# Kernel tuning notes

Measured on AMD Instinct MI355X. Metric: run time of the kernel, lower is better.

Reference implementation:

```python
import jax, jax.numpy as jnp
import numpy as np

RES = 64            # resolution -> RES*RES grid points
BW = 0.3            # kernel bandwidth
P = 2.0             # weight power
BOX = np.array([[-3.0, 3.0], [-3.0, 3.0]], dtype=np.float32)  # fixed_box [[min,max],[min,max]]


def _grid():
    # regular RES x RES grid over BOX, flattened to (M, 2)
    ax0 = np.linspace(BOX[0, 0], BOX[0, 1], RES, dtype=np.float32)
    ax1 = np.linspace(BOX[1, 0], BOX[1, 1], RES, dtype=np.float32)
    g0, g1 = np.meshgrid(ax0, ax1, indexing='ij')
    return jnp.asarray(np.stack([g0.ravel(), g1.ravel()], axis=-1))


def setup_inputs() -> dict:
    key = jax.random.key(0)
    k1, k2 = jax.random.split(key)
    Bs = jax.random.normal(k1, (4, 128, 16, 2), dtype=jnp.float32)  # birth corners (S,N,nB,2)
    Ds = jax.random.normal(k2, (4, 128, 16, 2), dtype=jnp.float32)  # death corners (S,N,nD,2)
    return {"Bs": Bs, "Ds": Ds}


def reference(Bs, Ds):
    # Bs: (S,N,nB,2) birth corners (pad with +inf), Ds: (S,N,nD,2) death corners (pad with -inf)
    x = _grid()                      # (M,2) grid points, M = RES*RES
    x0, x1 = x[:, 0], x[:, 1]

    # --- interleaving weights: dI0 per interval ---
    # pairwise relu(D - B).min(coords) -> max over (nB,nD); inf -> 0
    pw = jnp.min(jax.nn.relu(Ds[:, :, None, :, :] - Bs[:, :, :, None, :]), axis=-1)  # (S,N,nB,nD)
    w = jnp.max(pw, axis=(-1, -2))                                                   # (S,N)
    w = jnp.where(jnp.isfinite(w), w, 0.0)

    # --- distance from grid points to intervals ---
    # birth: min_k max_d (B[k,d] - x[d]); computed as elementwise max of the 2 coords
    db = jnp.min(
        jnp.maximum(Bs[..., 0][:, :, None, :] - x0[None, None, :, None],
                    Bs[..., 1][:, :, None, :] - x1[None, None, :, None]),
        axis=-1)                                                                     # (S,N,M)
    # death: min_k max_d (x[d] - D[k,d])
    dd = jnp.min(
        jnp.maximum(x0[None, None, :, None] - Ds[..., 0][:, :, None, :],
                    x1[None, None, :, None] - Ds[..., 1][:, :, None, :]),
        axis=-1)                                                                     # (S,N,M)
    dist = jnp.maximum(db, dd)                                                       # (S,N,M)

    # --- gaussian kernel, unsigned: exp(-0.5*(relu(dist)/bw)^2) * w^p, summed over intervals ---
    k = jnp.exp(-0.5 * (jax.nn.relu(dist) / BW) ** 2)
    img = jnp.sum(k * (w ** P)[:, :, None], axis=1)                                  # (S, M)
    return img  # flat vector per sample, shape (S, RES*RES)
```

## Files before the change

### kernel.cpp

```cpp
#include <hip/hip_runtime.h>
#include <math.h>

#define RES   64
#define NPTS  (RES * RES)
#define NB    4
#define NN    128
#define NP    16
#define STRIDE 36
#define PTS_PER_BLK 32
#define NCHUNK 32

__global__ __launch_bounds__(256)
void fused_kernel(const float* __restrict__ Bs, const float* __restrict__ Ds,
                  float* __restrict__ out) {
    __shared__ __align__(16) float sB[NN * STRIDE];
    __shared__ __align__(16) float sD[NN * STRIDE];
    __shared__ float sW2[NN];
    __shared__ float wp[2][NN];
    __shared__ float psum[NCHUNK][PTS_PER_BLK + 1];

    const int b    = blockIdx.x >> 7;
    const int pblk = blockIdx.x & 127;
    const int t    = threadIdx.x;

    const float4* gB = (const float4*)(Bs + (size_t)b * NN * NP * 2);
    const float4* gD = (const float4*)(Ds + (size_t)b * NN * NP * 2);
    #pragma unroll
    for (int r = 0; r < 4; ++r) {
        const int m   = t + 256 * r;
        const int off = (m >> 3) * STRIDE + (m & 7) * 4;
        *(float4*)(sB + off) = gB[m];
        *(float4*)(sD + off) = gD[m];
    }
    __syncthreads();

    {
        const int n  = t & 127;
        const int jh = t >> 7;
        const float4* B4 = (const float4*)(sB + n * STRIDE);
        const float4* D4 = (const float4*)(sD + n * STRIDE);
        float b0[NP], b1[NP];
        #pragma unroll
        for (int q = 0; q < 8; ++q) {
            const float4 f = B4[q];
            b0[2 * q] = f.x; b1[2 * q] = f.y;
            b0[2 * q + 1] = f.z; b1[2 * q + 1] = f.w;
        }
        float w = 0.0f;
        #pragma unroll
        for (int qq = 0; qq < 4; ++qq) {
            const float4 fd = D4[jh * 4 + qq];
            #pragma unroll
            for (int i = 0; i < NP; ++i) {
                w = fmaxf(w, fmaxf(fminf(fd.x - b0[i], fd.y - b1[i]), 0.0f));
                w = fmaxf(w, fmaxf(fminf(fd.z - b0[i], fd.w - b1[i]), 0.0f));
            }
        }
        wp[jh][n] = w;
    }
    __syncthreads();
    if (t < NN) {
        float wv = fmaxf(wp[0][t], wp[1][t]);
        if (!isfinite(wv)) wv = 0.0f;
        sW2[t] = wv * wv;
    }
    __syncthreads();

    const int g  = t & 7;
    const int c  = t >> 3;
    const int p0 = pblk * PTS_PER_BLK + 4 * g;
    const int i0 = p0 >> 6;
    const float x0 = -3.0f + 6.0f * (float)i0 / 63.0f;
    float x1v[4];
    #pragma unroll
    for (int j = 0; j < 4; ++j)
        x1v[j] = -3.0f + 6.0f * (float)((p0 + j) & 63) / 63.0f;

    const float cexp = -0.5f / (0.3f * 0.3f);
    float acc[4] = {0.0f, 0.0f, 0.0f, 0.0f};

    for (int k = 0; k < 4; ++k) {
        const int n = c + 32 * k;
        const float4* B4 = (const float4*)(sB + n * STRIDE);
        const float4* D4 = (const float4*)(sD + n * STRIDE);
        float db[4] = {1e30f, 1e30f, 1e30f, 1e30f};
        float dd[4] = {1e30f, 1e30f, 1e30f, 1e30f};
        #pragma unroll
        for (int q = 0; q < 8; ++q) {
            const float4 fb = B4[q];
            const float4 fd = D4[q];
            float s  = fb.x - x0;
            float sd = x0 - fd.x;
            #pragma unroll
            for (int j = 0; j < 4; ++j) {
                db[j] = fminf(db[j], fmaxf(s,  fb.y - x1v[j]));
                dd[j] = fminf(dd[j], fmaxf(sd, x1v[j] - fd.y));
            }
            s  = fb.z - x0;
            sd = x0 - fd.z;
            #pragma unroll
            for (int j = 0; j < 4; ++j) {
                db[j] = fminf(db[j], fmaxf(s,  fb.w - x1v[j]));
                dd[j] = fminf(dd[j], fmaxf(sd, x1v[j] - fd.w));
            }
        }
        const float w2n = sW2[n];
        #pragma unroll
        for (int j = 0; j < 4; ++j) {
            const float r = fmaxf(fmaxf(db[j], dd[j]), 0.0f);
            acc[j] = fmaf(__expf(cexp * r * r), w2n, acc[j]);
        }
    }

    #pragma unroll
    for (int j = 0; j < 4; ++j) psum[c][4 * g + j] = acc[j];
    __syncthreads();
    if (t < PTS_PER_BLK) {
        float s = 0.0f;
        #pragma unroll
        for (int q = 0; q < NCHUNK; ++q) s += psum[q][t];
        out[(size_t)b * NPTS + pblk * PTS_PER_BLK + t] = s;
    }
}

extern "C" void kernel_launch(void* const* d_in, const int* in_sizes, int n_in,
                              void* d_out, int out_size, void* d_ws, size_t ws_size,
                              hipStream_t stream) {
    const float* Bs = (const float*)d_in[0];
    const float* Ds = (const float*)d_in[1];
    float* out = (float*)d_out;
    fused_kernel<<<dim3(NB * (NPTS / PTS_PER_BLK)), dim3(256), 0, stream>>>(Bs, Ds, out);
}
```

Measured before the change: 62.45 us.

## Split weight computation into a pre-kernel and slice intervals across more blocks

The per-interval weights, which were recomputed redundantly in every block, are now computed once by a small separate kernel that also zeroes the output. The main kernel splits the 128 intervals of each sample into 4 slices, so it launches four times as many blocks, each loading only a quarter of the corner data into shared memory. Partial sums are combined with atomicAdd into global memory. This removes redundant weight computation and raises parallelism, at the cost of an extra launch, atomics, and a dependency on workspace memory.

```diff
diff --git a/kernel.cpp b/kernel.cpp
--- a/kernel.cpp
+++ b/kernel.cpp
@@ -8,66 +8,65 @@
 #define NP    16
 #define STRIDE 36
 #define PTS_PER_BLK 32
-#define NCHUNK 32
+#define NSLICE 4
+#define NCOMP_BLK 32
 
-__global__ __launch_bounds__(256)
-void fused_kernel(const float* __restrict__ Bs, const float* __restrict__ Ds,
-                  float* __restrict__ out) {
-    __shared__ __align__(16) float sB[NN * STRIDE];
-    __shared__ __align__(16) float sD[NN * STRIDE];
-    __shared__ float sW2[NN];
-    __shared__ float wp[2][NN];
-    __shared__ float psum[NCHUNK][PTS_PER_BLK + 1];
+__global__ __launch_bounds__(64)
+void w2_kernel(const float* __restrict__ Bs, const float* __restrict__ Ds,
+               float* __restrict__ w2, float* __restrict__ out) {
+    const int tid = blockIdx.x * 64 + threadIdx.x;
 
-    const int b    = blockIdx.x >> 7;
-    const int pblk = blockIdx.x & 127;
-    const int t    = threadIdx.x;
+    #pragma unroll
+    for (int k = 0; k < 32; ++k) out[tid + 512 * k] = 0.0f;
 
-    const float4* gB = (const float4*)(Bs + (size_t)b * NN * NP * 2);
-    const float4* gD = (const float4*)(Ds + (size_t)b * NN * NP * 2);
+    const float4* B4 = (const float4*)Bs + (size_t)tid * 8;
+    const float4* D4 = (const float4*)Ds + (size_t)tid * 8;
+    float b0[NP], b1[NP], d0[NP], d1[NP];
     #pragma unroll
-    for (int r = 0; r < 4; ++r) {
-        const int m   = t + 256 * r;
-        const int off = (m >> 3) * STRIDE + (m & 7) * 4;
-        *(float4*)(sB + off) = gB[m];
-        *(float4*)(sD + off) = gD[m];
+    for (int q = 0; q < 8; ++q) {
+        float4 f = B4[q];
+        b0[2*q] = f.x; b1[2*q] = f.y; b0[2*q+1] = f.z; b1[2*q+1] = f.w;
+        f = D4[q];
+        d0[2*q] = f.x; d1[2*q] = f.y; d0[2*q+1] = f.z; d1[2*q+1] = f.w;
+    }
+    float w = 0.0f;
+    #pragma unroll
+    for (int j = 0; j < NP; ++j) {
+        #pragma unroll
+        for (int i = 0; i < NP; ++i)
+            w = fmaxf(w, fminf(d0[j] - b0[i], d1[j] - b1[i]));
+    }
+    if (!isfinite(w)) w = 0.0f;
+    w2[tid] = w * w;
+}
+
+__global__ __launch_bounds__(256, 8)
+void main_kernel(const float* __restrict__ Bs, const float* __restrict__ Ds,
+                 const float* __restrict__ w2, float* __restrict__ out) {
+    __shared__ __align__(16) float sB[NCOMP_BLK * STRIDE];
+    __shared__ __align__(16) float sD[NCOMP_BLK * STRIDE];
+    __shared__ float psum[NCOMP_BLK][PTS_PER_BLK + 1];
+
+    const int bid   = blockIdx.x;
+    const int b     = bid >> 9;
+    const int pblk  = (bid >> 2) & 127;
+    const int slice = bid & 3;
+    const int t     = threadIdx.x;
+
+    {
+        const int comp0 = b * NN + slice * NCOMP_BLK;
+        const float4* gB = (const float4*)Bs + (size_t)comp0 * 8;
+        const float4* gD = (const float4*)Ds + (size_t)comp0 * 8;
+        const int off = (t >> 3) * STRIDE + (t & 7) * 4;
+        *(float4*)(sB + off) = gB[t];
+        *(float4*)(sD + off) = gD[t];
     }
     __syncthreads();
 
-    {
-        const int n  = t & 127;
-        const int jh = t >> 7;
-        const float4* B4 = (const float4*)(sB + n * STRIDE);
-        const float4* D4 = (const float4*)(sD + n * STRIDE);
-        float b0[NP], b1[NP];
-        #pragma unroll
-        for (int q = 0; q < 8; ++q) {
-            const float4 f = B4[q];
-            b0[2 * q] = f.x; b1[2 * q] = f.y;
-            b0[2 * q + 1] = f.z; b1[2 * q + 1] = f.w;
-        }
-        float w = 0.0f;
-        #pragma unroll
-        for (int qq = 0; qq < 4; ++qq) {
-            const float4 fd = D4[jh * 4 + qq];
-            #pragma unroll
-            for (int i = 0; i < NP; ++i) {
-                w = fmaxf(w, fmaxf(fminf(fd.x - b0[i], fd.y - b1[i]), 0.0f));
-                w = fmaxf(w, fmaxf(fminf(fd.z - b0[i], fd.w - b1[i]), 0.0f));
-            }
-        }
-        wp[jh][n] = w;
-    }
-    __syncthreads();
-    if (t < NN) {
-        float wv = fmaxf(wp[0][t], wp[1][t]);
-        if (!isfinite(wv)) wv = 0.0f;
-        sW2[t] = wv * wv;
-    }
-    __syncthreads();
+    const int g = t & 7;
+    const int c = t >> 3;
+    const float w2n = w2[b * NN + slice * NCOMP_BLK + c];
 
-    const int g  = t & 7;
-    const int c  = t >> 3;
     const int p0 = pblk * PTS_PER_BLK + 4 * g;
     const int i0 = p0 >> 6;
     const float x0 = -3.0f + 6.0f * (float)i0 / 63.0f;
@@ -76,50 +75,42 @@
     for (int j = 0; j < 4; ++j)
         x1v[j] = -3.0f + 6.0f * (float)((p0 + j) & 63) / 63.0f;
 
-    const float cexp = -0.5f / (0.3f * 0.3f);
-    float acc[4] = {0.0f, 0.0f, 0.0f, 0.0f};
-
-    for (int k = 0; k < 4; ++k) {
-        const int n = c + 32 * k;
-        const float4* B4 = (const float4*)(sB + n * STRIDE);
-        const float4* D4 = (const float4*)(sD + n * STRIDE);
-        float db[4] = {1e30f, 1e30f, 1e30f, 1e30f};
-        float dd[4] = {1e30f, 1e30f, 1e30f, 1e30f};
-        #pragma unroll
-        for (int q = 0; q < 8; ++q) {
-            const float4 fb = B4[q];
-            const float4 fd = D4[q];
-            float s  = fb.x - x0;
-            float sd = x0 - fd.x;
-            #pragma unroll
-            for (int j = 0; j < 4; ++j) {
-                db[j] = fminf(db[j], fmaxf(s,  fb.y - x1v[j]));
-                dd[j] = fminf(dd[j], fmaxf(sd, x1v[j] - fd.y));
-            }
-            s  = fb.z - x0;
-            sd = x0 - fd.z;
-            #pragma unroll
-            for (int j = 0; j < 4; ++j) {
-                db[j] = fminf(db[j], fmaxf(s,  fb.w - x1v[j]));
-                dd[j] = fminf(dd[j], fmaxf(sd, x1v[j] - fd.w));
-            }
-        }
-        const float w2n = sW2[n];
+    const float4* B4 = (const float4*)(sB + c * STRIDE);
+    const float4* D4 = (const float4*)(sD + c * STRIDE);
+    float db[4] = {1e30f, 1e30f, 1e30f, 1e30f};
+    float dd[4] = {1e30f, 1e30f, 1e30f, 1e30f};
+    #pragma unroll
+    for (int q = 0; q < 8; ++q) {
+        const float4 fb = B4[q];
+        const float4 fd = D4[q];
+        float s  = fb.x - x0;
+        float sd = x0 - fd.x;
         #pragma unroll
         for (int j = 0; j < 4; ++j) {
-            const float r = fmaxf(fmaxf(db[j], dd[j]), 0.0f);
-            acc[j] = fmaf(__expf(cexp * r * r), w2n, acc[j]);
+            db[j] = fminf(db[j], fmaxf(s,  fb.y - x1v[j]));
+            dd[j] = fminf(dd[j], fmaxf(sd, x1v[j] - fd.y));
+        }
+        s  = fb.z - x0;
+        sd = x0 - fd.z;
+        #pragma unroll
+        for (int j = 0; j < 4; ++j) {
+            db[j] = fminf(db[j], fmaxf(s,  fb.w - x1v[j]));
+            dd[j] = fminf(dd[j], fmaxf(sd, x1v[j] - fd.w));
         }
     }
+    const float cexp = -0.5f / (0.3f * 0.3f);
+    #pragma unroll
+    for (int j = 0; j < 4; ++j) {
+        const float r = fmaxf(fmaxf(db[j], dd[j]), 0.0f);
+        psum[c][4 * g + j] = __expf(cexp * r * r) * w2n;
+    }
+    __syncthreads();
 
-    #pragma unroll
-    for (int j = 0; j < 4; ++j) psum[c][4 * g + j] = acc[j];
-    __syncthreads();
     if (t < PTS_PER_BLK) {
-        float s = 0.0f;
+        float ssum = 0.0f;
         #pragma unroll
-        for (int q = 0; q < NCHUNK; ++q) s += psum[q][t];
-        out[(size_t)b * NPTS + pblk * PTS_PER_BLK + t] = s;
+        for (int q = 0; q < NCOMP_BLK; ++q) ssum += psum[q][t];
+        atomicAdd(&out[(size_t)b * NPTS + pblk * PTS_PER_BLK + t], ssum);
     }
 }
 
@@ -129,5 +120,8 @@
     const float* Bs = (const float*)d_in[0];
     const float* Ds = (const float*)d_in[1];
     float* out = (float*)d_out;
-    fused_kernel<<<dim3(NB * (NPTS / PTS_PER_BLK)), dim3(256), 0, stream>>>(Bs, Ds, out);
+    float* w2  = (float*)d_ws;
+
+    w2_kernel<<<dim3(8), dim3(64), 0, stream>>>(Bs, Ds, w2, out);
+    main_kernel<<<dim3(NB * 128 * NSLICE), dim3(256), 0, stream>>>(Bs, Ds, w2, out);
 }
```

Result: slower. 63.82 us (+2.2%).

## Use 1024-thread blocks with one interval per thread group and two-level reduction

Applied to the files above, without the earlier changes.

Block size grows from 256 to 1024 threads. Each group of 8 threads now owns one interval, so the per-thread loop over 4 intervals is gone. The weight computation is split across the 8 lanes and combined with xor shuffles, which removes a shared-memory round trip and one barrier. Partial sums go through a larger shared buffer with a two-level tree reduction. The aim is more parallelism and shorter per-thread serial chains, at the cost of more shared memory, more barriers on a large block, and lower occupancy limits per CU.

```diff
diff --git a/kernel.cpp b/kernel.cpp
--- a/kernel.cpp
+++ b/kernel.cpp
@@ -8,67 +8,57 @@
 #define NP    16
 #define STRIDE 36
 #define PTS_PER_BLK 32
-#define NCHUNK 32
 
-__global__ __launch_bounds__(256)
+__global__ __launch_bounds__(1024, 8)
 void fused_kernel(const float* __restrict__ Bs, const float* __restrict__ Ds,
                   float* __restrict__ out) {
     __shared__ __align__(16) float sB[NN * STRIDE];
     __shared__ __align__(16) float sD[NN * STRIDE];
     __shared__ float sW2[NN];
-    __shared__ float wp[2][NN];
-    __shared__ float psum[NCHUNK][PTS_PER_BLK + 1];
+    __shared__ float psum[NN][PTS_PER_BLK + 1];
+    __shared__ float pp[8][PTS_PER_BLK + 1];
 
-    const int b    = blockIdx.x >> 7;
-    const int pblk = blockIdx.x & 127;
+    const int bid  = blockIdx.x;
+    const int b    = bid >> 7;
+    const int pblk = bid & 127;
     const int t    = threadIdx.x;
 
-    const float4* gB = (const float4*)(Bs + (size_t)b * NN * NP * 2);
-    const float4* gD = (const float4*)(Ds + (size_t)b * NN * NP * 2);
-    #pragma unroll
-    for (int r = 0; r < 4; ++r) {
-        const int m   = t + 256 * r;
-        const int off = (m >> 3) * STRIDE + (m & 7) * 4;
-        *(float4*)(sB + off) = gB[m];
-        *(float4*)(sD + off) = gD[m];
+    {
+        const float4* gB = (const float4*)(Bs + (size_t)b * NN * NP * 2);
+        const float4* gD = (const float4*)(Ds + (size_t)b * NN * NP * 2);
+        const int off = (t >> 3) * STRIDE + (t & 7) * 4;
+        *(float4*)(sB + off) = gB[t];
+        *(float4*)(sD + off) = gD[t];
     }
     __syncthreads();
 
+    const int n   = t >> 3;
+    const int sub = t & 7;
+
+    const float4* B4 = (const float4*)(sB + n * STRIDE);
+    const float4* D4 = (const float4*)(sD + n * STRIDE);
+
     {
-        const int n  = t & 127;
-        const int jh = t >> 7;
-        const float4* B4 = (const float4*)(sB + n * STRIDE);
-        const float4* D4 = (const float4*)(sD + n * STRIDE);
-        float b0[NP], b1[NP];
+        const float4 fd = D4[sub];
+        float w = 0.0f;
         #pragma unroll
         for (int q = 0; q < 8; ++q) {
-            const float4 f = B4[q];
-            b0[2 * q] = f.x; b1[2 * q] = f.y;
-            b0[2 * q + 1] = f.z; b1[2 * q + 1] = f.w;
+            const float4 fb = B4[q];
+            w = fmaxf(w, fminf(fd.x - fb.x, fd.y - fb.y));
+            w = fmaxf(w, fminf(fd.x - fb.z, fd.y - fb.w));
+            w = fmaxf(w, fminf(fd.z - fb.x, fd.w - fb.y));
+            w = fmaxf(w, fminf(fd.z - fb.z, fd.w - fb.w));
         }
-        float w = 0.0f;
-        #pragma unroll
-        for (int qq = 0; qq < 4; ++qq) {
-            const float4 fd = D4[jh * 4 + qq];
-            #pragma unroll
-            for (int i = 0; i < NP; ++i) {
-                w = fmaxf(w, fmaxf(fminf(fd.x - b0[i], fd.y - b1[i]), 0.0f));
-                w = fmaxf(w, fmaxf(fminf(fd.z - b0[i], fd.w - b1[i]), 0.0f));
-            }
+        w = fmaxf(w, __shfl_xor(w, 1));
+        w = fmaxf(w, __shfl_xor(w, 2));
+        w = fmaxf(w, __shfl_xor(w, 4));
+        if (sub == 0) {
+            if (!isfinite(w)) w = 0.0f;
+            sW2[n] = w * w;
         }
-        wp[jh][n] = w;
     }
-    __syncthreads();
-    if (t < NN) {
-        float wv = fmaxf(wp[0][t], wp[1][t]);
-        if (!isfinite(wv)) wv = 0.0f;
-        sW2[t] = wv * wv;
-    }
-    __syncthreads();
 
-    const int g  = t & 7;
-    const int c  = t >> 3;
-    const int p0 = pblk * PTS_PER_BLK + 4 * g;
+    const int p0 = pblk * PTS_PER_BLK + 4 * sub;
     const int i0 = p0 >> 6;
     const float x0 = -3.0f + 6.0f * (float)i0 / 63.0f;
     float x1v[4];
@@ -76,49 +66,52 @@
     for (int j = 0; j < 4; ++j)
         x1v[j] = -3.0f + 6.0f * (float)((p0 + j) & 63) / 63.0f;
 
-    const float cexp = -0.5f / (0.3f * 0.3f);
-    float acc[4] = {0.0f, 0.0f, 0.0f, 0.0f};
-
-    for (int k = 0; k < 4; ++k) {
-        const int n = c + 32 * k;
-        const float4* B4 = (const float4*)(sB + n * STRIDE);
-        const float4* D4 = (const float4*)(sD + n * STRIDE);
-        float db[4] = {1e30f, 1e30f, 1e30f, 1e30f};
-        float dd[4] = {1e30f, 1e30f, 1e30f, 1e30f};
-        #pragma unroll
-        for (int q = 0; q < 8; ++q) {
-            const float4 fb = B4[q];
-            const float4 fd = D4[q];
-            float s  = fb.x - x0;
-            float sd = x0 - fd.x;
-            #pragma unroll
-            for (int j = 0; j < 4; ++j) {
-                db[j] = fminf(db[j], fmaxf(s,  fb.y - x1v[j]));
-                dd[j] = fminf(dd[j], fmaxf(sd, x1v[j] - fd.y));
-            }
-            s  = fb.z - x0;
-            sd = x0 - fd.z;
-            #pragma unroll
-            for (int j = 0; j < 4; ++j) {
-                db[j] = fminf(db[j], fmaxf(s,  fb.w - x1v[j]));
-                dd[j] = fminf(dd[j], fmaxf(sd, x1v[j] - fd.w));
-            }
-        }
-        const float w2n = sW2[n];
+    float db[4] = {1e30f, 1e30f, 1e30f, 1e30f};
+    float dd[4] = {1e30f, 1e30f, 1e30f, 1e30f};
+    #pragma unroll 4
+    for (int q = 0; q < 8; ++q) {
+        const float4 fb = B4[q];
+        const float4 fd = D4[q];
+        float s  = fb.x - x0;
+        float sd = x0 - fd.x;
         #pragma unroll
         for (int j = 0; j < 4; ++j) {
-            const float r = fmaxf(fmaxf(db[j], dd[j]), 0.0f);
-            acc[j] = fmaf(__expf(cexp * r * r), w2n, acc[j]);
+            db[j] = fminf(db[j], fmaxf(s,  fb.y - x1v[j]));
+            dd[j] = fminf(dd[j], fmaxf(sd, x1v[j] - fd.y));
+        }
+        s  = fb.z - x0;
+        sd = x0 - fd.z;
+        #pragma unroll
+        for (int j = 0; j < 4; ++j) {
+            db[j] = fminf(db[j], fmaxf(s,  fb.w - x1v[j]));
+            dd[j] = fminf(dd[j], fmaxf(sd, x1v[j] - fd.w));
         }
     }
 
+    __syncthreads();
+    const float w2n = sW2[n];
+    const float cexp = -0.5f / (0.3f * 0.3f);
     #pragma unroll
-    for (int j = 0; j < 4; ++j) psum[c][4 * g + j] = acc[j];
+    for (int j = 0; j < 4; ++j) {
+        const float r = fmaxf(fmaxf(db[j], dd[j]), 0.0f);
+        psum[n][4 * sub + j] = __expf(cexp * r * r) * w2n;
+    }
+    __syncthreads();
+
+    if (t < 256) {
+        const int p   = t & 31;
+        const int oct = t >> 5;
+        float s = 0.0f;
+        #pragma unroll
+        for (int m = 0; m < 16; ++m)
+            s += psum[oct * 16 + m][p];
+        pp[oct][p] = s;
+    }
     __syncthreads();
     if (t < PTS_PER_BLK) {
         float s = 0.0f;
         #pragma unroll
-        for (int q = 0; q < NCHUNK; ++q) s += psum[q][t];
+        for (int q = 0; q < 8; ++q) s += pp[q][t];
         out[(size_t)b * NPTS + pblk * PTS_PER_BLK + t] = s;
     }
 }
@@ -129,5 +122,5 @@
     const float* Bs = (const float*)d_in[0];
     const float* Ds = (const float*)d_in[1];
     float* out = (float*)d_out;
-    fused_kernel<<<dim3(NB * (NPTS / PTS_PER_BLK)), dim3(256), 0, stream>>>(Bs, Ds, out);
+    fused_kernel<<<dim3(NB * 128), dim3(1024), 0, stream>>>(Bs, Ds, out);
 }
```

After: 61.74 us (median of 2 runs). No clear change (-1.1%).
